# Kernel optimization log

Measured on AMD Instinct MI355X. Metric: run time of the kernel, lower is better.

Reference implementation:

```python
import jax, jax.numpy as jnp
import numpy as np

N, E = 50000, 800000
IN_DIM, HID, HEADS, OUT_DIM = 128, 64, 4, 64
NEG_SLOPE = 0.2


def add_self_loops(edge_index, n):
    loops = jnp.arange(n, dtype=edge_index.dtype)
    return jnp.concatenate([edge_index, jnp.stack([loops, loops])], axis=1)


def gat_layer(x, edge_index, W, att_src, att_dst, bias, heads, ch, concat):
    n = x.shape[0]
    xp = (x @ W).reshape(n, heads, ch)                       # [N,H,C]
    s_src = jnp.sum(xp * att_src, axis=-1)                   # [N,H]
    s_dst = jnp.sum(xp * att_dst, axis=-1)                   # [N,H]
    src, dst = edge_index[0], edge_index[1]
    e = jax.nn.leaky_relu(s_src[src] + s_dst[dst], NEG_SLOPE)  # [E,H]
    # segment softmax over incoming edges of each destination node
    m = jax.ops.segment_max(e, dst, num_segments=n)
    e = jnp.exp(e - m[dst])
    denom = jax.ops.segment_sum(e, dst, num_segments=n)
    alpha = e / (denom[dst] + 1e-16)                         # [E,H]
    out = jax.ops.segment_sum(xp[src] * alpha[:, :, None], dst, num_segments=n)  # [N,H,C]
    out = out.reshape(n, heads * ch) if concat else out.mean(axis=1)
    return out + bias


def setup_inputs() -> dict:
    key = jax.random.key(0)
    ks = jax.random.split(key, 10)
    glorot = lambda k, shape: jax.random.normal(k, shape, jnp.float32) * np.sqrt(2.0 / (shape[0] + shape[-1]))
    return {
        "x": jax.random.normal(ks[0], (N, IN_DIM), jnp.float32),
        "edge_index": jax.random.randint(ks[1], (2, E), 0, N, jnp.int32),
        "W1": glorot(ks[2], (IN_DIM, HEADS * HID)),
        "att_src1": glorot(ks[3], (HEADS, HID)),
        "att_dst1": glorot(ks[4], (HEADS, HID)),
        "bias1": jnp.zeros((HEADS * HID,), jnp.float32),
        "W2": glorot(ks[5], (HEADS * HID, OUT_DIM)),
        "att_src2": glorot(ks[6], (1, OUT_DIM)),
        "att_dst2": glorot(ks[7], (1, OUT_DIM)),
        "bias2": jnp.zeros((OUT_DIM,), jnp.float32),
    }


def reference(x, edge_index, W1, att_src1, att_dst1, bias1, W2, att_src2, att_dst2, bias2):
    ei = add_self_loops(edge_index, x.shape[0])
    h = gat_layer(x, ei, W1, att_src1, att_dst1, bias1, HEADS, HID, concat=True)
    h = jax.nn.relu(h)
    out = gat_layer(h, ei, W2, att_src2, att_dst2, bias2, 1, OUT_DIM, concat=False)
    return out
```

## Files before the change

kernel.cpp:

```cpp
#include <hip/hip_runtime.h>
#include <hip/hip_bf16.h>
#include <hip/hip_fp16.h>

#define NODES 50000
#define NEDGE 800000
#define NE2   850000
#define INDIM 128
#define F1    256
#define HEADS 4
#define HID   64
#define OUTD  64
#define MTILES 3125

#define NB   196
#define PB   196
#define EPB  4096
#define TOTH (NB*PB)

typedef _Float16 f16;
typedef _Float16 f16x8 __attribute__((ext_vector_type(8)));
typedef float    f32x4 __attribute__((ext_vector_type(4)));

__global__ void k_hist(const int* __restrict__ ei, int* __restrict__ blkhist,
                       const float* __restrict__ W1, const float* __restrict__ W2,
                       f16* __restrict__ W1p, f16* __restrict__ W2p)
{
    const int b = blockIdx.x, t = threadIdx.x;
    if (b < PB) {
        __shared__ int h[NB];
        for (int i = t; i < NB; i += 256) h[i] = 0;
        __syncthreads();
        const int e0 = b * EPB;
        const int eend = min(e0 + EPB, NEDGE);
        for (int i = e0 + t; i < eend; i += 256) {
            int d = ei[NEDGE + i];
            atomicAdd(&h[d >> 8], 1);
        }
        __syncthreads();
        for (int i = t; i < NB; i += 256) blkhist[i * PB + b] = h[i];
    } else {
        int idx = (b - PB) * 256 + t;
        if (idx < 32768) {
            int j = idx & 7, l = (idx >> 3) & 63, fi = idx >> 9;
            int kb = fi & 3, ct = fi >> 2;
            int k = kb * 32 + (l >> 4) * 8 + j;
            int col = ct * 16 + (l & 15);
            W1p[idx] = (f16)W1[k * F1 + col];
        } else {
            int i2 = idx - 32768;
            int j = i2 & 7, l = (i2 >> 3) & 63, fi = i2 >> 9;
            int kb = fi & 7, ct = fi >> 3;
            int k = kb * 32 + (l >> 4) * 8 + j;
            int col = ct * 16 + (l & 15);
            W2p[i2] = (f16)W2[k * OUTD + col];
        }
    }
}

__global__ void k_scanR(int* __restrict__ blkhist, int* __restrict__ rowtot)
{
    __shared__ int sh[256];
    const int q = blockIdx.x, t = threadIdx.x;
    int v = (t < PB) ? blkhist[q * PB + t] : 0;
    sh[t] = v; __syncthreads();
    for (int off = 1; off < 256; off <<= 1) {
        int tv = (t >= off) ? sh[t - off] : 0;
        __syncthreads();
        sh[t] += tv;
        __syncthreads();
    }
    if (t < PB) blkhist[q * PB + t] = sh[t] - v;
    if (t == 255) rowtot[q] = sh[255];
}

__global__ void k_part(const int* __restrict__ ei, const int* __restrict__ blkhist,
                       const int* __restrict__ rowtot, unsigned* __restrict__ staged)
{
    const int b = blockIdx.x, t = threadIdx.x;
    __shared__ int sS[256];
    __shared__ int cur[NB];
    int v = (t < NB) ? rowtot[t] : 0;
    sS[t] = v; __syncthreads();
    for (int off = 1; off < 256; off <<= 1) {
        int tv = (t >= off) ? sS[t - off] : 0;
        __syncthreads();
        sS[t] += tv;
        __syncthreads();
    }
    if (t < NB) cur[t] = (sS[t] - v) + blkhist[t * PB + b];
    __syncthreads();
    const int e0 = b * EPB;
    const int eend = min(e0 + EPB, NEDGE);
    for (int i = e0 + t; i < eend; i += 256) {
        int sN = ei[i];
        int d  = ei[NEDGE + i];
        int pos = atomicAdd(&cur[d >> 8], 1);
        staged[pos] = (unsigned)sN | ((unsigned)(d & 255) << 16);
    }
}

__global__ void k_bucket(const unsigned* __restrict__ staged,
                         const int* __restrict__ rowtot,
                         int* __restrict__ row_ptr, int* __restrict__ csr_src)
{
    const int q = blockIdx.x, t = threadIdx.x;
    const int wv = t >> 6, lane = t & 63;
    __shared__ int ssum[4];
    __shared__ int cnt[256];
    __shared__ int sh[256];
    int pv = (t < q) ? rowtot[t] : 0;
#pragma unroll
    for (int off = 32; off; off >>= 1) pv += __shfl_xor(pv, off);
    if (lane == 0) ssum[wv] = pv;
    cnt[t] = 0;
    __syncthreads();
    const int estart = ssum[0] + ssum[1] + ssum[2] + ssum[3];
    const int eend   = estart + rowtot[q];
    const int nodebase = q * 256;
    const int nn = min(256, NODES - nodebase);
    const int csrbase = estart + nodebase;

    for (int i = estart + t; i < eend; i += 256)
        atomicAdd(&cnt[staged[i] >> 16], 1);
    __syncthreads();
    int v = cnt[t];
    sh[t] = v;
    __syncthreads();
    for (int off = 1; off < 256; off <<= 1) {
        int tv = (t >= off) ? sh[t - off] : 0;
        __syncthreads();
        sh[t] += tv;
        __syncthreads();
    }
    int excl = sh[t] - v;
    if (t < nn) {
        int r = csrbase + excl + t;
        row_ptr[nodebase + t] = r;
        csr_src[r] = nodebase + t;
        cnt[t] = excl + t + 1;
    }
    __syncthreads();
    for (int i = estart + t; i < eend; i += 256) {
        unsigned u = staged[i];
        int pos = atomicAdd(&cnt[u >> 16], 1);
        csr_src[csrbase + pos] = (int)(u & 0xFFFFu);
    }
    if (q == NB - 1 && t == 0) row_ptr[NODES] = NE2;
}

__global__ __launch_bounds__(256) void k_gemm1m(
    const float* __restrict__ x, const f16* __restrict__ W1p,
    const float* __restrict__ as1, const float* __restrict__ ad1,
    f16* __restrict__ xp1h, float* __restrict__ ssrc, float* __restrict__ sdst)
{
    const int wv = threadIdx.x >> 6, lane = threadIdx.x & 63;
    const int l15 = lane & 15, quad = lane >> 4;
    const int rowtile = blockIdx.x * 4 + wv;
    if (rowtile >= MTILES) return;
    const int rowbase = rowtile * 16;

    f16x8 afrag[4];
    const float* xrow = x + (rowbase + l15) * INDIM + quad * 8;
#pragma unroll
    for (int kb = 0; kb < 4; ++kb) {
        float4 u0 = *(const float4*)(xrow + kb * 32);
        float4 u1 = *(const float4*)(xrow + kb * 32 + 4);
        f16x8 a;
        a[0] = (f16)u0.x; a[1] = (f16)u0.y; a[2] = (f16)u0.z; a[3] = (f16)u0.w;
        a[4] = (f16)u1.x; a[5] = (f16)u1.y; a[6] = (f16)u1.z; a[7] = (f16)u1.w;
        afrag[kb] = a;
    }

    const f16x8* Wf = (const f16x8*)W1p;
    f32x4 acc[16];
#pragma unroll
    for (int ct = 0; ct < 16; ++ct) acc[ct] = (f32x4){0.f, 0.f, 0.f, 0.f};
#pragma unroll
    for (int ct = 0; ct < 16; ++ct) {
#pragma unroll
        for (int kb = 0; kb < 4; ++kb) {
            f16x8 b = Wf[(ct * 4 + kb) * 64 + lane];
            acc[ct] = __builtin_amdgcn_mfma_f32_16x16x32_f16(afrag[kb], b, acc[ct], 0, 0, 0);
        }
    }
    const int orow = rowbase + quad * 4;
#pragma unroll
    for (int ct = 0; ct < 16; ++ct) {
#pragma unroll
        for (int r = 0; r < 4; ++r)
            xp1h[(orow + r) * F1 + ct * 16 + l15] = (f16)acc[ct][r];
    }
    float ps[4][4], pd[4][4];
#pragma unroll
    for (int h = 0; h < 4; ++h)
#pragma unroll
        for (int r = 0; r < 4; ++r) { ps[h][r] = 0.f; pd[h][r] = 0.f; }
#pragma unroll
    for (int ct = 0; ct < 16; ++ct) {
        float av = as1[ct * 16 + l15];
        float dv = ad1[ct * 16 + l15];
        int h = ct >> 2;
#pragma unroll
        for (int r = 0; r < 4; ++r) {
            ps[h][r] = fmaf(acc[ct][r], av, ps[h][r]);
            pd[h][r] = fmaf(acc[ct][r], dv, pd[h][r]);
        }
    }
#pragma unroll
    for (int off = 8; off; off >>= 1) {
#pragma unroll
        for (int h = 0; h < 4; ++h)
#pragma unroll
            for (int r = 0; r < 4; ++r) {
                ps[h][r] += __shfl_xor(ps[h][r], off);
                pd[h][r] += __shfl_xor(pd[h][r], off);
            }
    }
    if (l15 == 0) {
#pragma unroll
        for (int r = 0; r < 4; ++r) {
            int row = orow + r;
            float4 vs = {ps[0][r], ps[1][r], ps[2][r], ps[3][r]};
            float4 vd = {pd[0][r], pd[1][r], pd[2][r], pd[3][r]};
            ((float4*)ssrc)[row] = vs;
            ((float4*)sdst)[row] = vd;
        }
    }
}

__global__ __launch_bounds__(256) void k_agg1(
    const int* __restrict__ row_ptr, const int* __restrict__ csr_src,
    const float* __restrict__ ssrc, const float* __restrict__ sdst,
    const f16* __restrict__ xp1h, const float* __restrict__ bias,
    f16* __restrict__ hbuf)
{
    const int wv = threadIdx.x >> 6, l = threadIdx.x & 63;
    const int n = blockIdx.x * 4 + wv;
    const int eq = l & 15, ph = l >> 4;
    const int g  = l >> 4, sub = l & 15;
    const int sel_lo = (sub >> 3) << 4;
    const int sel_hi = (2 + (sub >> 3)) << 4;
    const float sd = sdst[n * HEADS + ph];
    const int jbeg = row_ptr[n], jend = row_ptr[n + 1];
    const f16x8* xv = (const f16x8*)xp1h;

    float den = 0.f;
    float alo[8] = {0.f,0.f,0.f,0.f,0.f,0.f,0.f,0.f};
    float ahi[8] = {0.f,0.f,0.f,0.f,0.f,0.f,0.f,0.f};
    for (int base = jbeg; base < jend; base += 16) {
        int c = jend - base; if (c > 16) c = 16;
        int s = 0; float ex = 0.f;
        if (eq < c) {
            s = csr_src[base + eq];
            float e = ssrc[s * HEADS + ph] + sd;
            e = e > 0.f ? e : 0.2f * e;
            ex = __expf(e);
        }
        den += ex;
        int p = 0;
        for (; p + 7 < c; p += 8) {
            int ea = p + g, eb = p + 4 + g;
            int   sa  = __shfl(s, ea),          sb  = __shfl(s, eb);
            float aal = __shfl(ex, ea | sel_lo), aah = __shfl(ex, ea | sel_hi);
            float abl = __shfl(ex, eb | sel_lo), abh = __shfl(ex, eb | sel_hi);
            f16x8 va0 = xv[sa * 32 + sub];
            f16x8 va1 = xv[sa * 32 + sub + 16];
            f16x8 vb0 = xv[sb * 32 + sub];
            f16x8 vb1 = xv[sb * 32 + sub + 16];
#pragma unroll
            for (int j = 0; j < 8; ++j) {
                alo[j] = fmaf(aal, (float)va0[j], alo[j]);
                ahi[j] = fmaf(aah, (float)va1[j], ahi[j]);
            }
#pragma unroll
            for (int j = 0; j < 8; ++j) {
                alo[j] = fmaf(abl, (float)vb0[j], alo[j]);
                ahi[j] = fmaf(abh, (float)vb1[j], ahi[j]);
            }
        }
        for (; p < c; p += 4) {
            int ea = p + g;
            int   sa  = __shfl(s, ea);
            float aal = __shfl(ex, ea | sel_lo), aah = __shfl(ex, ea | sel_hi);
            f16x8 va0 = xv[sa * 32 + sub];
            f16x8 va1 = xv[sa * 32 + sub + 16];
#pragma unroll
            for (int j = 0; j < 8; ++j) {
                alo[j] = fmaf(aal, (float)va0[j], alo[j]);
                ahi[j] = fmaf(aah, (float)va1[j], ahi[j]);
            }
        }
    }
#pragma unroll
    for (int off = 8; off; off >>= 1) den += __shfl_xor(den, off);
    const float dl = __shfl(den, sel_lo);
    const float dh = __shfl(den, sel_hi);
    const float rdl = 1.f / (dl + 1e-16f);
    const float rdh = 1.f / (dh + 1e-16f);
#pragma unroll
    for (int j = 0; j < 8; ++j) {
        alo[j] += __shfl_xor(alo[j], 16); alo[j] += __shfl_xor(alo[j], 32);
        ahi[j] += __shfl_xor(ahi[j], 16); ahi[j] += __shfl_xor(ahi[j], 32);
    }
    if (g == 0) {
        const float4* b4 = (const float4*)bias;
        float4 bl0 = b4[sub * 2],        bl1 = b4[sub * 2 + 1];
        float4 bh0 = b4[(sub + 16) * 2], bh1 = b4[(sub + 16) * 2 + 1];
        f16x8 olo, ohi;
        float v;
        v = fmaf(alo[0], rdl, bl0.x); olo[0] = (f16)(v > 0.f ? v : 0.f);
        v = fmaf(alo[1], rdl, bl0.y); olo[1] = (f16)(v > 0.f ? v : 0.f);
        v = fmaf(alo[2], rdl, bl0.z); olo[2] = (f16)(v > 0.f ? v : 0.f);
        v = fmaf(alo[3], rdl, bl0.w); olo[3] = (f16)(v > 0.f ? v : 0.f);
        v = fmaf(alo[4], rdl, bl1.x); olo[4] = (f16)(v > 0.f ? v : 0.f);
        v = fmaf(alo[5], rdl, bl1.y); olo[5] = (f16)(v > 0.f ? v : 0.f);
        v = fmaf(alo[6], rdl, bl1.z); olo[6] = (f16)(v > 0.f ? v : 0.f);
        v = fmaf(alo[7], rdl, bl1.w); olo[7] = (f16)(v > 0.f ? v : 0.f);
        v = fmaf(ahi[0], rdh, bh0.x); ohi[0] = (f16)(v > 0.f ? v : 0.f);
        v = fmaf(ahi[1], rdh, bh0.y); ohi[1] = (f16)(v > 0.f ? v : 0.f);
        v = fmaf(ahi[2], rdh, bh0.z); ohi[2] = (f16)(v > 0.f ? v : 0.f);
        v = fmaf(ahi[3], rdh, bh0.w); ohi[3] = (f16)(v > 0.f ? v : 0.f);
        v = fmaf(ahi[4], rdh, bh1.x); ohi[4] = (f16)(v > 0.f ? v : 0.f);
        v = fmaf(ahi[5], rdh, bh1.y); ohi[5] = (f16)(v > 0.f ? v : 0.f);
        v = fmaf(ahi[6], rdh, bh1.z); ohi[6] = (f16)(v > 0.f ? v : 0.f);
        v = fmaf(ahi[7], rdh, bh1.w); ohi[7] = (f16)(v > 0.f ? v : 0.f);
        ((f16x8*)hbuf)[n * 32 + sub] = olo;
        ((f16x8*)hbuf)[n * 32 + sub + 16] = ohi;
    }
}

__global__ __launch_bounds__(256) void k_gemm2m(
    const f16* __restrict__ hbuf, const f16* __restrict__ W2p,
    const float* __restrict__ as2, const float* __restrict__ ad2,
    f16* __restrict__ xp2h, float* __restrict__ ssrc, float* __restrict__ sdst)
{
    const int wv = threadIdx.x >> 6, lane = threadIdx.x & 63;
    const int l15 = lane & 15, quad = lane >> 4;
    const int rowtile = blockIdx.x * 4 + wv;
    if (rowtile >= MTILES) return;
    const int rowbase = rowtile * 16;

    const f16x8* Wf = (const f16x8*)W2p;
    f32x4 acc[4];
#pragma unroll
    for (int ct = 0; ct < 4; ++ct) acc[ct] = (f32x4){0.f, 0.f, 0.f, 0.f};
    const f16* hrow = hbuf + (rowbase + l15) * F1 + quad * 8;
#pragma unroll
    for (int kb = 0; kb < 8; ++kb) {
        f16x8 a = *(const f16x8*)(hrow + kb * 32);
#pragma unroll
        for (int ct = 0; ct < 4; ++ct) {
            f16x8 b = Wf[(ct * 8 + kb) * 64 + lane];
            acc[ct] = __builtin_amdgcn_mfma_f32_16x16x32_f16(a, b, acc[ct], 0, 0, 0);
        }
    }
    const int orow = rowbase + quad * 4;
#pragma unroll
    for (int ct = 0; ct < 4; ++ct) {
#pragma unroll
        for (int r = 0; r < 4; ++r)
            xp2h[(orow + r) * OUTD + ct * 16 + l15] = (f16)acc[ct][r];
    }
    float ps[4] = {0.f,0.f,0.f,0.f}, pd[4] = {0.f,0.f,0.f,0.f};
#pragma unroll
    for (int ct = 0; ct < 4; ++ct) {
        float av = as2[ct * 16 + l15];
        float dv = ad2[ct * 16 + l15];
#pragma unroll
        for (int r = 0; r < 4; ++r) {
            ps[r] = fmaf(acc[ct][r], av, ps[r]);
            pd[r] = fmaf(acc[ct][r], dv, pd[r]);
        }
    }
#pragma unroll
    for (int off = 8; off; off >>= 1) {
#pragma unroll
        for (int r = 0; r < 4; ++r) {
            ps[r] += __shfl_xor(ps[r], off);
            pd[r] += __shfl_xor(pd[r], off);
        }
    }
    if (l15 == 0) {
#pragma unroll
        for (int r = 0; r < 4; ++r) {
            ssrc[orow + r] = ps[r];
            sdst[orow + r] = pd[r];
        }
    }
}

__global__ __launch_bounds__(256) void k_agg2(
    const int* __restrict__ row_ptr, const int* __restrict__ csr_src,
    const float* __restrict__ ssrc, const float* __restrict__ sdst,
    const f16* __restrict__ xp2h, const float* __restrict__ bias,
    float* __restrict__ out)
{
    const int wv = threadIdx.x >> 6, l = threadIdx.x & 63;
    const int n = blockIdx.x * 4 + wv;
    const int grp = l >> 3, sub = l & 7;
    const float sd = sdst[n];
    const int jbeg = row_ptr[n], jend = row_ptr[n + 1];
    const f16x8* xv = (const f16x8*)xp2h;

    float den = 0.f;
    float acc[8] = {0.f,0.f,0.f,0.f,0.f,0.f,0.f,0.f};
    for (int base = jbeg; base < jend; base += 64) {
        int c = jend - base; if (c > 64) c = 64;
        int s = 0; float ex = 0.f;
        if (l < c) {
            s = csr_src[base + l];
            float e = ssrc[s] + sd;
            e = e > 0.f ? e : 0.2f * e;
            ex = __expf(e);
        }
        den += ex;
        int i = 0;
        for (; 8 * (i + 1) < c; i += 2) {
            int ea = 8 * i + grp, eb = 8 * i + 8 + grp;
            int   sa = __shfl(s, ea),  sb = __shfl(s, eb);
            float aa = __shfl(ex, ea), ab = __shfl(ex, eb);
            f16x8 va = xv[sa * 8 + sub];
            f16x8 vb = xv[sb * 8 + sub];
#pragma unroll
            for (int j = 0; j < 8; ++j) acc[j] = fmaf(aa, (float)va[j], acc[j]);
#pragma unroll
            for (int j = 0; j < 8; ++j) acc[j] = fmaf(ab, (float)vb[j], acc[j]);
        }
        for (; 8 * i < c; ++i) {
            int eidx = 8 * i + grp;
            int   se = __shfl(s, eidx);
            float ae = __shfl(ex, eidx);
            f16x8 v = xv[se * 8 + sub];
#pragma unroll
            for (int j = 0; j < 8; ++j) acc[j] = fmaf(ae, (float)v[j], acc[j]);
        }
    }
#pragma unroll
    for (int off = 32; off; off >>= 1) den += __shfl_xor(den, off);
    const float rd = 1.f / (den + 1e-16f);
#pragma unroll
    for (int j = 0; j < 8; ++j) {
        acc[j] += __shfl_xor(acc[j], 8);
        acc[j] += __shfl_xor(acc[j], 16);
        acc[j] += __shfl_xor(acc[j], 32);
    }
    if (grp == 0) {
        const float4* b4 = (const float4*)bias;
        float4 ba = b4[sub * 2], bb = b4[sub * 2 + 1];
        float4 o0, o1;
        o0.x = fmaf(acc[0], rd, ba.x); o0.y = fmaf(acc[1], rd, ba.y);
        o0.z = fmaf(acc[2], rd, ba.z); o0.w = fmaf(acc[3], rd, ba.w);
        o1.x = fmaf(acc[4], rd, bb.x); o1.y = fmaf(acc[5], rd, bb.y);
        o1.z = fmaf(acc[6], rd, bb.z); o1.w = fmaf(acc[7], rd, bb.w);
        float4* ov = (float4*)out + n * 16 + sub * 2;
        ov[0] = o0; ov[1] = o1;
    }
}

extern "C" void kernel_launch(void* const* d_in, const int* in_sizes, int n_in,
                              void* d_out, int out_size, void* d_ws, size_t ws_size,
                              hipStream_t stream)
{
    (void)in_sizes; (void)n_in; (void)out_size; (void)ws_size;
    const float* x   = (const float*)d_in[0];
    const int*   ei  = (const int*)d_in[1];
    const float* W1  = (const float*)d_in[2];
    const float* as1 = (const float*)d_in[3];
    const float* ad1 = (const float*)d_in[4];
    const float* b1  = (const float*)d_in[5];
    const float* W2  = (const float*)d_in[6];
    const float* as2 = (const float*)d_in[7];
    const float* ad2 = (const float*)d_in[8];
    const float* b2  = (const float*)d_in[9];
    float* out = (float*)d_out;

    f16* xp1h    = (f16*)d_ws;
    f16* hbuf    = xp1h + (size_t)NODES * F1;
    f16* W1p     = hbuf + (size_t)NODES * F1;
    f16* W2p     = W1p + 32768;
    float* ssrc1 = (float*)(W2p + 16384);
    float* sdst1 = ssrc1 + (size_t)NODES * HEADS;
    float* ssrc2 = sdst1 + (size_t)NODES * HEADS;
    float* sdst2 = ssrc2 + (size_t)NODES;
    int* row_ptr = (int*)(sdst2 + (size_t)NODES);
    int* blkhist = row_ptr + NODES + 1;
    int* rowtot  = blkhist + TOTH;
    int* csr_src = rowtot + NB;
    unsigned* staged = (unsigned*)(csr_src + NE2);
    f16* xp2h    = xp1h;

    k_hist<<<PB + 192, 256, 0, stream>>>(ei, blkhist, W1, W2, W1p, W2p);
    k_scanR<<<NB, 256, 0, stream>>>(blkhist, rowtot);
    k_part<<<PB, 256, 0, stream>>>(ei, blkhist, rowtot, staged);
    k_bucket<<<NB, 256, 0, stream>>>(staged, rowtot, row_ptr, csr_src);

    k_gemm1m<<<(MTILES + 3) / 4, 256, 0, stream>>>(x, W1p, as1, ad1,
                                                   xp1h, ssrc1, sdst1);
    k_agg1<<<NODES / 4, 256, 0, stream>>>(row_ptr, csr_src, ssrc1, sdst1,
                                          xp1h, b1, hbuf);

    k_gemm2m<<<(MTILES + 3) / 4, 256, 0, stream>>>(hbuf, W2p, as2, ad2,
                                                   xp2h, ssrc2, sdst2);
    k_agg2<<<NODES / 4, 256, 0, stream>>>(row_ptr, csr_src, ssrc2, sdst2,
                                          xp2h, b2, out);
}
```

Measured before the change: 236.5 us.

## Fuse CSR bucket pass with first GEMM and presort edges by source

Merges the bucket/CSR-building kernel and the first-layer GEMM into a single launch, with the first NB blocks building CSR and the rest doing GEMM tiles, so the two independent stages overlap and one launch is removed. Within the bucket blocks, each bucket's edges are first counting-sorted by the source's high byte in shared memory, so per-destination neighbor lists end up roughly ordered by source. That gives later gathers better locality. The cost is extra shared memory (24KB) in every block, which may lower occupancy for the GEMM blocks, plus an extra sort pass.

```diff
diff --git a/kernel.cpp b/kernel.cpp
--- a/kernel.cpp
+++ b/kernel.cpp
@@ -15,7 +15,8 @@
 #define NB   196
 #define PB   196
 #define EPB  4096
-#define TOTH (NB*PB)
+#define CAP  6144
+#define G1B  782
 
 typedef _Float16 f16;
 typedef _Float16 f16x8 __attribute__((ext_vector_type(8)));
@@ -99,63 +100,103 @@
     }
 }
 
-__global__ void k_bucket(const unsigned* __restrict__ staged,
-                         const int* __restrict__ rowtot,
-                         int* __restrict__ row_ptr, int* __restrict__ csr_src)
-{
-    const int q = blockIdx.x, t = threadIdx.x;
-    const int wv = t >> 6, lane = t & 63;
-    __shared__ int ssum[4];
-    __shared__ int cnt[256];
-    __shared__ int sh[256];
-    int pv = (t < q) ? rowtot[t] : 0;
-#pragma unroll
-    for (int off = 32; off; off >>= 1) pv += __shfl_xor(pv, off);
-    if (lane == 0) ssum[wv] = pv;
-    cnt[t] = 0;
-    __syncthreads();
-    const int estart = ssum[0] + ssum[1] + ssum[2] + ssum[3];
-    const int eend   = estart + rowtot[q];
-    const int nodebase = q * 256;
-    const int nn = min(256, NODES - nodebase);
-    const int csrbase = estart + nodebase;
-
-    for (int i = estart + t; i < eend; i += 256)
-        atomicAdd(&cnt[staged[i] >> 16], 1);
-    __syncthreads();
-    int v = cnt[t];
-    sh[t] = v;
-    __syncthreads();
-    for (int off = 1; off < 256; off <<= 1) {
-        int tv = (t >= off) ? sh[t - off] : 0;
-        __syncthreads();
-        sh[t] += tv;
-        __syncthreads();
-    }
-    int excl = sh[t] - v;
-    if (t < nn) {
-        int r = csrbase + excl + t;
-        row_ptr[nodebase + t] = r;
-        csr_src[r] = nodebase + t;
-        cnt[t] = excl + t + 1;
-    }
-    __syncthreads();
-    for (int i = estart + t; i < eend; i += 256) {
-        unsigned u = staged[i];
-        int pos = atomicAdd(&cnt[u >> 16], 1);
-        csr_src[csrbase + pos] = (int)(u & 0xFFFFu);
-    }
-    if (q == NB - 1 && t == 0) row_ptr[NODES] = NE2;
-}
-
-__global__ __launch_bounds__(256) void k_gemm1m(
+__global__ __launch_bounds__(256) void k_bg(
+    const unsigned* __restrict__ staged, const int* __restrict__ rowtot,
+    int* __restrict__ row_ptr, int* __restrict__ csr_src,
     const float* __restrict__ x, const f16* __restrict__ W1p,
     const float* __restrict__ as1, const float* __restrict__ ad1,
     f16* __restrict__ xp1h, float* __restrict__ ssrc, float* __restrict__ sdst)
 {
+    if (blockIdx.x < NB) {
+        __shared__ unsigned sorted2[CAP];
+        __shared__ int bin[256];
+        __shared__ int cnt[256];
+        __shared__ int sh[256];
+        __shared__ int ssum[4];
+        const int q = blockIdx.x, t = threadIdx.x;
+        const int wv = t >> 6, lane = t & 63;
+        int pv = (t < q) ? rowtot[t] : 0;
+#pragma unroll
+        for (int off = 32; off; off >>= 1) pv += __shfl_xor(pv, off);
+        if (lane == 0) ssum[wv] = pv;
+        cnt[t] = 0; bin[t] = 0;
+        __syncthreads();
+        const int estart = ssum[0] + ssum[1] + ssum[2] + ssum[3];
+        const int m = rowtot[q];
+        const int nodebase = q * 256;
+        const int nn = min(256, NODES - nodebase);
+        const int csrbase = estart + nodebase;
+
+        const bool dosort = (m <= CAP);
+        if (dosort) {
+            for (int i = t; i < m; i += 256)
+                atomicAdd(&bin[(staged[estart + i] & 0xFFFFu) >> 8], 1);
+            __syncthreads();
+            int bv = bin[t];
+            sh[t] = bv;
+            __syncthreads();
+            for (int off = 1; off < 256; off <<= 1) {
+                int tv = (t >= off) ? sh[t - off] : 0;
+                __syncthreads();
+                sh[t] += tv;
+                __syncthreads();
+            }
+            bin[t] = sh[t] - bv;
+            __syncthreads();
+            for (int i = t; i < m; i += 256) {
+                unsigned u = staged[estart + i];
+                int p = atomicAdd(&bin[(u & 0xFFFFu) >> 8], 1);
+                sorted2[p] = u;
+            }
+            __syncthreads();
+        }
+
+        if (dosort) {
+            for (int i = t; i < m; i += 256)
+                atomicAdd(&cnt[sorted2[i] >> 16], 1);
+        } else {
+            for (int i = t; i < m; i += 256)
+                atomicAdd(&cnt[staged[estart + i] >> 16], 1);
+        }
+        __syncthreads();
+        int v = cnt[t];
+        sh[t] = v;
+        __syncthreads();
+        for (int off = 1; off < 256; off <<= 1) {
+            int tv = (t >= off) ? sh[t - off] : 0;
+            __syncthreads();
+            sh[t] += tv;
+            __syncthreads();
+        }
+        int excl = sh[t] - v;
+        __syncthreads();
+        if (t < nn) {
+            int r = csrbase + excl + t;
+            row_ptr[nodebase + t] = r;
+            csr_src[r] = nodebase + t;
+            cnt[t] = excl + t + 1;
+        }
+        __syncthreads();
+        if (dosort) {
+            for (int i = t; i < m; i += 256) {
+                unsigned u = sorted2[i];
+                int pos = atomicAdd(&cnt[u >> 16], 1);
+                csr_src[csrbase + pos] = (int)(u & 0xFFFFu);
+            }
+        } else {
+            for (int i = t; i < m; i += 256) {
+                unsigned u = staged[estart + i];
+                int pos = atomicAdd(&cnt[u >> 16], 1);
+                csr_src[csrbase + pos] = (int)(u & 0xFFFFu);
+            }
+        }
+        if (q == NB - 1 && t == 0) row_ptr[NODES] = NE2;
+        return;
+    }
+
     const int wv = threadIdx.x >> 6, lane = threadIdx.x & 63;
     const int l15 = lane & 15, quad = lane >> 4;
-    const int rowtile = blockIdx.x * 4 + wv;
+    const int rowtile = (blockIdx.x - NB) * 4 + wv;
     if (rowtile >= MTILES) return;
     const int rowbase = rowtile * 16;
 
@@ -484,7 +525,7 @@
     float* sdst2 = ssrc2 + (size_t)NODES;
     int* row_ptr = (int*)(sdst2 + (size_t)NODES);
     int* blkhist = row_ptr + NODES + 1;
-    int* rowtot  = blkhist + TOTH;
+    int* rowtot  = blkhist + NB * PB;
     int* csr_src = rowtot + NB;
     unsigned* staged = (unsigned*)(csr_src + NE2);
     f16* xp2h    = xp1h;
@@ -492,10 +533,10 @@
     k_hist<<<PB + 192, 256, 0, stream>>>(ei, blkhist, W1, W2, W1p, W2p);
     k_scanR<<<NB, 256, 0, stream>>>(blkhist, rowtot);
     k_part<<<PB, 256, 0, stream>>>(ei, blkhist, rowtot, staged);
-    k_bucket<<<NB, 256, 0, stream>>>(staged, rowtot, row_ptr, csr_src);
-
-    k_gemm1m<<<(MTILES + 3) / 4, 256, 0, stream>>>(x, W1p, as1, ad1,
-                                                   xp1h, ssrc1, sdst1);
+
+    k_bg<<<NB + G1B, 256, 0, stream>>>(staged, rowtot, row_ptr, csr_src,
+                                       x, W1p, as1, ad1, xp1h, ssrc1, sdst1);
+
     k_agg1<<<NODES / 4, 256, 0, stream>>>(row_ptr, csr_src, ssrc1, sdst1,
                                           xp1h, b1, hbuf);
 
```

Result: faster. 228.4 us (-3.4%).

## Merge bucket and GEMM1 launches; restructure aggregation loops for direct per-edge gathers

Applied to the files above, without the earlier changes.

Fuses the CSR bucket kernel and the first GEMM into one launch, with the first NB blocks doing bucketing and the rest doing GEMM, so the two independent stages overlap and one launch is saved. Both aggregation kernels drop the chunked shuffle-broadcast scheme. Each lane group now loads its own edges' source indices and scores directly, four edges per iteration, so more gathers are in flight. In layer 1 the four head scores are read as a single float4. The cost is redundant exp/score work across lanes and more registers, which may lower occupancy.

```diff
diff --git a/kernel.cpp b/kernel.cpp
--- a/kernel.cpp
+++ b/kernel.cpp
@@ -15,11 +15,16 @@
 #define NB   196
 #define PB   196
 #define EPB  4096
-#define TOTH (NB*PB)
+#define G1B  782
 
 typedef _Float16 f16;
 typedef _Float16 f16x8 __attribute__((ext_vector_type(8)));
 typedef float    f32x4 __attribute__((ext_vector_type(4)));
+
+__device__ __forceinline__ float lrelu_exp(float e) {
+    e = e > 0.f ? e : 0.2f * e;
+    return __expf(e);
+}
 
 __global__ void k_hist(const int* __restrict__ ei, int* __restrict__ blkhist,
                        const float* __restrict__ W1, const float* __restrict__ W2,
@@ -99,63 +104,64 @@
     }
 }
 
-__global__ void k_bucket(const unsigned* __restrict__ staged,
-                         const int* __restrict__ rowtot,
-                         int* __restrict__ row_ptr, int* __restrict__ csr_src)
-{
-    const int q = blockIdx.x, t = threadIdx.x;
-    const int wv = t >> 6, lane = t & 63;
-    __shared__ int ssum[4];
-    __shared__ int cnt[256];
-    __shared__ int sh[256];
-    int pv = (t < q) ? rowtot[t] : 0;
-#pragma unroll
-    for (int off = 32; off; off >>= 1) pv += __shfl_xor(pv, off);
-    if (lane == 0) ssum[wv] = pv;
-    cnt[t] = 0;
-    __syncthreads();
-    const int estart = ssum[0] + ssum[1] + ssum[2] + ssum[3];
-    const int eend   = estart + rowtot[q];
-    const int nodebase = q * 256;
-    const int nn = min(256, NODES - nodebase);
-    const int csrbase = estart + nodebase;
-
-    for (int i = estart + t; i < eend; i += 256)
-        atomicAdd(&cnt[staged[i] >> 16], 1);
-    __syncthreads();
-    int v = cnt[t];
-    sh[t] = v;
-    __syncthreads();
-    for (int off = 1; off < 256; off <<= 1) {
-        int tv = (t >= off) ? sh[t - off] : 0;
-        __syncthreads();
-        sh[t] += tv;
-        __syncthreads();
-    }
-    int excl = sh[t] - v;
-    if (t < nn) {
-        int r = csrbase + excl + t;
-        row_ptr[nodebase + t] = r;
-        csr_src[r] = nodebase + t;
-        cnt[t] = excl + t + 1;
-    }
-    __syncthreads();
-    for (int i = estart + t; i < eend; i += 256) {
-        unsigned u = staged[i];
-        int pos = atomicAdd(&cnt[u >> 16], 1);
-        csr_src[csrbase + pos] = (int)(u & 0xFFFFu);
-    }
-    if (q == NB - 1 && t == 0) row_ptr[NODES] = NE2;
-}
-
-__global__ __launch_bounds__(256) void k_gemm1m(
+__global__ __launch_bounds__(256) void k_bg(
+    const unsigned* __restrict__ staged, const int* __restrict__ rowtot,
+    int* __restrict__ row_ptr, int* __restrict__ csr_src,
     const float* __restrict__ x, const f16* __restrict__ W1p,
     const float* __restrict__ as1, const float* __restrict__ ad1,
     f16* __restrict__ xp1h, float* __restrict__ ssrc, float* __restrict__ sdst)
 {
+    if (blockIdx.x < NB) {
+        __shared__ int cnt[256];
+        __shared__ int sh[256];
+        __shared__ int ssum[4];
+        const int q = blockIdx.x, t = threadIdx.x;
+        const int wv = t >> 6, lane = t & 63;
+        int pv = (t < q) ? rowtot[t] : 0;
+#pragma unroll
+        for (int off = 32; off; off >>= 1) pv += __shfl_xor(pv, off);
+        if (lane == 0) ssum[wv] = pv;
+        cnt[t] = 0;
+        __syncthreads();
+        const int estart = ssum[0] + ssum[1] + ssum[2] + ssum[3];
+        const int eend   = estart + rowtot[q];
+        const int nodebase = q * 256;
+        const int nn = min(256, NODES - nodebase);
+        const int csrbase = estart + nodebase;
+
+        for (int i = estart + t; i < eend; i += 256)
+            atomicAdd(&cnt[staged[i] >> 16], 1);
+        __syncthreads();
+        int v = cnt[t];
+        sh[t] = v;
+        __syncthreads();
+        for (int off = 1; off < 256; off <<= 1) {
+            int tv = (t >= off) ? sh[t - off] : 0;
+            __syncthreads();
+            sh[t] += tv;
+            __syncthreads();
+        }
+        int excl = sh[t] - v;
+        __syncthreads();
+        if (t < nn) {
+            int r = csrbase + excl + t;
+            row_ptr[nodebase + t] = r;
+            csr_src[r] = nodebase + t;
+            cnt[t] = excl + t + 1;
+        }
+        __syncthreads();
+        for (int i = estart + t; i < eend; i += 256) {
+            unsigned u = staged[i];
+            int pos = atomicAdd(&cnt[u >> 16], 1);
+            csr_src[csrbase + pos] = (int)(u & 0xFFFFu);
+        }
+        if (q == NB - 1 && t == 0) row_ptr[NODES] = NE2;
+        return;
+    }
+
     const int wv = threadIdx.x >> 6, lane = threadIdx.x & 63;
     const int l15 = lane & 15, quad = lane >> 4;
-    const int rowtile = blockIdx.x * 4 + wv;
+    const int rowtile = (blockIdx.x - NB) * 4 + wv;
     if (rowtile >= MTILES) return;
     const int rowbase = rowtile * 16;
 
@@ -236,67 +242,68 @@
 {
     const int wv = threadIdx.x >> 6, l = threadIdx.x & 63;
     const int n = blockIdx.x * 4 + wv;
-    const int eq = l & 15, ph = l >> 4;
-    const int g  = l >> 4, sub = l & 15;
-    const int sel_lo = (sub >> 3) << 4;
-    const int sel_hi = (2 + (sub >> 3)) << 4;
-    const float sd = sdst[n * HEADS + ph];
+    const int g = l >> 4, sub = l & 15;
+    const int hlo = sub >> 3;
+    const float sdl = sdst[n * HEADS + hlo];
+    const float sdh = sdst[n * HEADS + 2 + hlo];
     const int jbeg = row_ptr[n], jend = row_ptr[n + 1];
     const f16x8* xv = (const f16x8*)xp1h;
-
-    float den = 0.f;
+    const float4* sv = (const float4*)ssrc;
+
+    float denl = 0.f, denh = 0.f;
     float alo[8] = {0.f,0.f,0.f,0.f,0.f,0.f,0.f,0.f};
     float ahi[8] = {0.f,0.f,0.f,0.f,0.f,0.f,0.f,0.f};
-    for (int base = jbeg; base < jend; base += 16) {
-        int c = jend - base; if (c > 16) c = 16;
-        int s = 0; float ex = 0.f;
-        if (eq < c) {
-            s = csr_src[base + eq];
-            float e = ssrc[s * HEADS + ph] + sd;
-            e = e > 0.f ? e : 0.2f * e;
-            ex = __expf(e);
-        }
-        den += ex;
-        int p = 0;
-        for (; p + 7 < c; p += 8) {
-            int ea = p + g, eb = p + 4 + g;
-            int   sa  = __shfl(s, ea),          sb  = __shfl(s, eb);
-            float aal = __shfl(ex, ea | sel_lo), aah = __shfl(ex, ea | sel_hi);
-            float abl = __shfl(ex, eb | sel_lo), abh = __shfl(ex, eb | sel_hi);
-            f16x8 va0 = xv[sa * 32 + sub];
-            f16x8 va1 = xv[sa * 32 + sub + 16];
-            f16x8 vb0 = xv[sb * 32 + sub];
-            f16x8 vb1 = xv[sb * 32 + sub + 16];
-#pragma unroll
-            for (int j = 0; j < 8; ++j) {
-                alo[j] = fmaf(aal, (float)va0[j], alo[j]);
-                ahi[j] = fmaf(aah, (float)va1[j], ahi[j]);
-            }
-#pragma unroll
-            for (int j = 0; j < 8; ++j) {
-                alo[j] = fmaf(abl, (float)vb0[j], alo[j]);
-                ahi[j] = fmaf(abh, (float)vb1[j], ahi[j]);
-            }
-        }
-        for (; p < c; p += 4) {
-            int ea = p + g;
-            int   sa  = __shfl(s, ea);
-            float aal = __shfl(ex, ea | sel_lo), aah = __shfl(ex, ea | sel_hi);
-            f16x8 va0 = xv[sa * 32 + sub];
-            f16x8 va1 = xv[sa * 32 + sub + 16];
-#pragma unroll
-            for (int j = 0; j < 8; ++j) {
-                alo[j] = fmaf(aal, (float)va0[j], alo[j]);
-                ahi[j] = fmaf(aah, (float)va1[j], ahi[j]);
-            }
-        }
-    }
-#pragma unroll
-    for (int off = 8; off; off >>= 1) den += __shfl_xor(den, off);
-    const float dl = __shfl(den, sel_lo);
-    const float dh = __shfl(den, sel_hi);
-    const float rdl = 1.f / (dl + 1e-16f);
-    const float rdh = 1.f / (dh + 1e-16f);
+
+    for (int e = jbeg + g; e < jend; e += 16) {
+        const int e1 = e + 4, e2 = e + 8, e3 = e + 12;
+        const bool v1 = e1 < jend, v2 = e2 < jend, v3 = e3 < jend;
+        int s0 = csr_src[e];
+        int s1 = v1 ? csr_src[e1] : 0;
+        int s2 = v2 ? csr_src[e2] : 0;
+        int s3 = v3 ? csr_src[e3] : 0;
+        float4 q0 = sv[s0];
+        float4 q1 = sv[s1];
+        float4 q2 = sv[s2];
+        float4 q3 = sv[s3];
+        f16x8 w0l = xv[s0 * 32 + sub], w0h = xv[s0 * 32 + sub + 16];
+        f16x8 w1l = xv[s1 * 32 + sub], w1h = xv[s1 * 32 + sub + 16];
+        f16x8 w2l = xv[s2 * 32 + sub], w2h = xv[s2 * 32 + sub + 16];
+        f16x8 w3l = xv[s3 * 32 + sub], w3h = xv[s3 * 32 + sub + 16];
+        float x0l = lrelu_exp((hlo ? q0.y : q0.x) + sdl);
+        float x0h = lrelu_exp((hlo ? q0.w : q0.z) + sdh);
+        float x1l = v1 ? lrelu_exp((hlo ? q1.y : q1.x) + sdl) : 0.f;
+        float x1h = v1 ? lrelu_exp((hlo ? q1.w : q1.z) + sdh) : 0.f;
+        float x2l = v2 ? lrelu_exp((hlo ? q2.y : q2.x) + sdl) : 0.f;
+        float x2h = v2 ? lrelu_exp((hlo ? q2.w : q2.z) + sdh) : 0.f;
+        float x3l = v3 ? lrelu_exp((hlo ? q3.y : q3.x) + sdl) : 0.f;
+        float x3h = v3 ? lrelu_exp((hlo ? q3.w : q3.z) + sdh) : 0.f;
+        denl += (x0l + x1l) + (x2l + x3l);
+        denh += (x0h + x1h) + (x2h + x3h);
+#pragma unroll
+        for (int j = 0; j < 8; ++j) {
+            alo[j] = fmaf(x0l, (float)w0l[j], alo[j]);
+            ahi[j] = fmaf(x0h, (float)w0h[j], ahi[j]);
+        }
+#pragma unroll
+        for (int j = 0; j < 8; ++j) {
+            alo[j] = fmaf(x1l, (float)w1l[j], alo[j]);
+            ahi[j] = fmaf(x1h, (float)w1h[j], ahi[j]);
+        }
+#pragma unroll
+        for (int j = 0; j < 8; ++j) {
+            alo[j] = fmaf(x2l, (float)w2l[j], alo[j]);
+            ahi[j] = fmaf(x2h, (float)w2h[j], ahi[j]);
+        }
+#pragma unroll
+        for (int j = 0; j < 8; ++j) {
+            alo[j] = fmaf(x3l, (float)w3l[j], alo[j]);
+            ahi[j] = fmaf(x3h, (float)w3h[j], ahi[j]);
+        }
+    }
+    denl += __shfl_xor(denl, 16); denl += __shfl_xor(denl, 32);
+    denh += __shfl_xor(denh, 16); denh += __shfl_xor(denh, 32);
+    const float rdl = 1.f / (denl + 1e-16f);
+    const float rdh = 1.f / (denh + 1e-16f);
 #pragma unroll
     for (int j = 0; j < 8; ++j) {
         alo[j] += __shfl_xor(alo[j], 16); alo[j] += __shfl_xor(alo[j], 32);
@@ -404,39 +411,38 @@
 
     float den = 0.f;
     float acc[8] = {0.f,0.f,0.f,0.f,0.f,0.f,0.f,0.f};
-    for (int base = jbeg; base < jend; base += 64) {
-        int c = jend - base; if (c > 64) c = 64;
-        int s = 0; float ex = 0.f;
-        if (l < c) {
-            s = csr_src[base + l];
-            float e = ssrc[s] + sd;
-            e = e > 0.f ? e : 0.2f * e;
-            ex = __expf(e);
-        }
-        den += ex;
-        int i = 0;
-        for (; 8 * (i + 1) < c; i += 2) {
-            int ea = 8 * i + grp, eb = 8 * i + 8 + grp;
-            int   sa = __shfl(s, ea),  sb = __shfl(s, eb);
-            float aa = __shfl(ex, ea), ab = __shfl(ex, eb);
-            f16x8 va = xv[sa * 8 + sub];
-            f16x8 vb = xv[sb * 8 + sub];
-#pragma unroll
-            for (int j = 0; j < 8; ++j) acc[j] = fmaf(aa, (float)va[j], acc[j]);
-#pragma unroll
-            for (int j = 0; j < 8; ++j) acc[j] = fmaf(ab, (float)vb[j], acc[j]);
-        }
-        for (; 8 * i < c; ++i) {
-            int eidx = 8 * i + grp;
-            int   se = __shfl(s, eidx);
-            float ae = __shfl(ex, eidx);
-            f16x8 v = xv[se * 8 + sub];
-#pragma unroll
-            for (int j = 0; j < 8; ++j) acc[j] = fmaf(ae, (float)v[j], acc[j]);
-        }
-    }
-#pragma unroll
-    for (int off = 32; off; off >>= 1) den += __shfl_xor(den, off);
+    for (int e = jbeg + grp; e < jend; e += 32) {
+        const int e1 = e + 8, e2 = e + 16, e3 = e + 24;
+        const bool v1 = e1 < jend, v2 = e2 < jend, v3 = e3 < jend;
+        int s0 = csr_src[e];
+        int s1 = v1 ? csr_src[e1] : 0;
+        int s2 = v2 ? csr_src[e2] : 0;
+        int s3 = v3 ? csr_src[e3] : 0;
+        float c0 = ssrc[s0];
+        float c1 = ssrc[s1];
+        float c2 = ssrc[s2];
+        float c3 = ssrc[s3];
+        f16x8 w0 = xv[s0 * 8 + sub];
+        f16x8 w1 = xv[s1 * 8 + sub];
+        f16x8 w2 = xv[s2 * 8 + sub];
+        f16x8 w3 = xv[s3 * 8 + sub];
+        float x0 = lrelu_exp(c0 + sd);
+        float x1 = v1 ? lrelu_exp(c1 + sd) : 0.f;
+        float x2 = v2 ? lrelu_exp(c2 + sd) : 0.f;
+        float x3 = v3 ? lrelu_exp(c3 + sd) : 0.f;
+        den += (x0 + x1) + (x2 + x3);
+#pragma unroll
+        for (int j = 0; j < 8; ++j) acc[j] = fmaf(x0, (float)w0[j], acc[j]);
+#pragma unroll
+        for (int j = 0; j < 8; ++j) acc[j] = fmaf(x1, (float)w1[j], acc[j]);
+#pragma unroll
+        for (int j = 0; j < 8; ++j) acc[j] = fmaf(x2, (float)w2[j], acc[j]);
+#pragma unroll
+        for (int j = 0; j < 8; ++j) acc[j] = fmaf(x3, (float)w3[j], acc[j]);
+    }
+    den += __shfl_xor(den, 8);
+    den += __shfl_xor(den, 16);
+    den += __shfl_xor(den, 32);
     const float rd = 1.f / (den + 1e-16f);
 #pragma unroll
     for (int j = 0; j < 8; ++j) {
@@ -484,7 +490,7 @@
     float* sdst2 = ssrc2 + (size_t)NODES;
     int* row_ptr = (int*)(sdst2 + (size_t)NODES);
     int* blkhist = row_ptr + NODES + 1;
-    int* rowtot  = blkhist + TOTH;
+    int* rowtot  = blkhist + NB * PB;
     int* csr_src = rowtot + NB;
     unsigned* staged = (unsigned*)(csr_src + NE2);
     f16* xp2h    = xp1h;
@@ -492,10 +498,10 @@
     k_hist<<<PB + 192, 256, 0, stream>>>(ei, blkhist, W1, W2, W1p, W2p);
     k_scanR<<<NB, 256, 0, stream>>>(blkhist, rowtot);
     k_part<<<PB, 256, 0, stream>>>(ei, blkhist, rowtot, staged);
-    k_bucket<<<NB, 256, 0, stream>>>(staged, rowtot, row_ptr, csr_src);
-
-    k_gemm1m<<<(MTILES + 3) / 4, 256, 0, stream>>>(x, W1p, as1, ad1,
-                                                   xp1h, ssrc1, sdst1);
+
+    k_bg<<<NB + G1B, 256, 0, stream>>>(staged, rowtot, row_ptr, csr_src,
+                                       x, W1p, as1, ad1, xp1h, ssrc1, sdst1);
+
     k_agg1<<<NODES / 4, 256, 0, stream>>>(row_ptr, csr_src, ssrc1, sdst1,
                                           xp1h, b1, hbuf);
 
```

Measured after the change: 228.5 us. 1.03x faster.
